# Kernel optimization log

Hardware: AMD Instinct MI355X
Metric: run time of the kernel (lower is better)

## Reference

```python
import jax, jax.numpy as jnp
import numpy as np

N_NODES = 50000
EPS = 1e-5


def gcn_conv(x, edge_index, edge_weight, W, b, n):
    # PyG GCNConv: h = x @ W; out[dst] += norm * h[src]; out += b
    # with self-loops (weight 1) and symmetric normalization D^-1/2 A D^-1/2.
    src, dst = edge_index[0], edge_index[1]
    loop = jnp.arange(n)
    src_all = jnp.concatenate([src, loop])            # [E+N]
    dst_all = jnp.concatenate([dst, loop])
    w_all = jnp.concatenate([edge_weight, jnp.ones((n,), x.dtype)])
    deg = jax.ops.segment_sum(w_all, dst_all, num_segments=n)
    dinv = jnp.where(deg > 0, jax.lax.rsqrt(jnp.maximum(deg, 1e-30)), 0.0)
    norm = dinv[src_all] * w_all * dinv[dst_all]      # [E+N]
    h = x @ W                                         # [N, out]
    msg = h[src_all] * norm[:, None]                  # [E+N, out]
    return jax.ops.segment_sum(msg, dst_all, num_segments=n) + b


def setup_inputs() -> dict:
    key = jax.random.key(0)
    ks = jax.random.split(key, 8)
    nfeat, nhid, nout = 1024, 256, 256
    E = 800000
    x = jax.random.normal(ks[0], (N_NODES, nfeat), dtype=jnp.float32)
    edge_index = jax.random.randint(ks[1], (2, E), 0, N_NODES, dtype=jnp.int64)
    edge_weight = jax.random.uniform(ks[2], (E,), dtype=jnp.float32)
    W1 = jax.random.normal(ks[3], (nfeat, nhid), dtype=jnp.float32) / np.sqrt(nfeat)
    b1 = jnp.zeros((nhid,), jnp.float32)
    W2 = jax.random.normal(ks[4], (nhid, nout), dtype=jnp.float32) / np.sqrt(nhid)
    b2 = jnp.zeros((nout,), jnp.float32)
    bn_gamma = jnp.ones((nout,), jnp.float32)
    bn_beta = jnp.zeros((nout,), jnp.float32)
    ln_gamma = jnp.ones((nout,), jnp.float32)
    ln_beta = jnp.zeros((nout,), jnp.float32)
    return {"x": x, "edge_index": edge_index, "edge_weight": edge_weight,
            "W1": W1, "b1": b1, "W2": W2, "b2": b2,
            "bn_gamma": bn_gamma, "bn_beta": bn_beta,
            "ln_gamma": ln_gamma, "ln_beta": ln_beta}


def reference(x, edge_index, edge_weight, W1, b1, W2, b2,
              bn_gamma, bn_beta, ln_gamma, ln_beta):
    n = x.shape[0]
    # dropout is identity in eval mode
    h = jax.nn.relu(gcn_conv(x, edge_index, edge_weight, W1, b1, n))
    h = jax.nn.relu(gcn_conv(h, edge_index, edge_weight, W2, b2, n))
    # BatchNorm1d (training-mode batch statistics, biased variance)
    mu = jnp.mean(h, axis=0)
    var = jnp.mean((h - mu) ** 2, axis=0)
    h = (h - mu) * jax.lax.rsqrt(var + EPS) * bn_gamma + bn_beta
    # LayerNorm over feature dim
    lmu = jnp.mean(h, axis=-1, keepdims=True)
    lvar = jnp.mean((h - lmu) ** 2, axis=-1, keepdims=True)
    return (h - lmu) * jax.lax.rsqrt(lvar + EPS) * ln_gamma + ln_beta
```

## Files before the change

kernel.cpp:

```cpp
#include <hip/hip_runtime.h>


typedef __attribute__((ext_vector_type(4))) float f32x4;
typedef __attribute__((ext_vector_type(8))) _Float16 f16x8;
typedef __attribute__((ext_vector_type(4))) _Float16 f16x4;

#define NN 50000
#define NF 1024
#define NH 256

__global__ __launch_bounds__(256) void deg_count(const int* __restrict__ ei,
    const float* __restrict__ ew, float* __restrict__ deg, int* __restrict__ cnt, int E)
{
    int e = blockIdx.x * 256 + threadIdx.x;
    if (e >= E) return;
    int d = ei[E + e];
    atomicAdd(&deg[d], ew[e]);
    atomicAdd(&cnt[d], 1);
}

__global__ __launch_bounds__(256) void dinv_k(const float* __restrict__ deg,
    float* __restrict__ dinv, int n)
{
    int i = blockIdx.x * 256 + threadIdx.x;
    if (i < n) dinv[i] = rsqrtf(deg[i] + 1.0f);
}

__global__ __launch_bounds__(512) void scan_a(const int* __restrict__ cnt,
    int* __restrict__ excl, int* __restrict__ bsum, int n)
{
    __shared__ int sm[512];
    int t = threadIdx.x, g = blockIdx.x * 512 + t;
    int v = (g < n) ? cnt[g] : 0;
    sm[t] = v;
    __syncthreads();
    for (int d = 1; d < 512; d <<= 1) {
        int x = (t >= d) ? sm[t - d] : 0;
        __syncthreads();
        sm[t] += x;
        __syncthreads();
    }
    if (g < n) excl[g] = sm[t] - v;
    if (t == 511) bsum[blockIdx.x] = sm[511];
}

__global__ __launch_bounds__(128) void scan_b(int* __restrict__ bsum, int nb)
{
    __shared__ int sm[128];
    int t = threadIdx.x;
    int v = (t < nb) ? bsum[t] : 0;
    sm[t] = v;
    __syncthreads();
    for (int d = 1; d < 128; d <<= 1) {
        int x = (t >= d) ? sm[t - d] : 0;
        __syncthreads();
        sm[t] += x;
        __syncthreads();
    }
    if (t < nb) bsum[t] = sm[t] - v;
}

__global__ __launch_bounds__(256) void scan_c(const int* __restrict__ excl,
    const int* __restrict__ bsum, int* __restrict__ offs, int n, int E)
{
    int g = blockIdx.x * 256 + threadIdx.x;
    if (g < n) offs[g] = excl[g] + bsum[g >> 9];
    else if (g == n) offs[n] = E;
}

__global__ __launch_bounds__(256) void scatter_k(const int* __restrict__ ei,
    const float* __restrict__ ew, const int* __restrict__ offs,
    int* __restrict__ cursor, const float* __restrict__ dinv,
    int* __restrict__ csrc, float* __restrict__ cwv, int E)
{
    int e = blockIdx.x * 256 + threadIdx.x;
    if (e >= E) return;
    int s = ei[e], d = ei[E + e];
    int pos = offs[d] + atomicAdd(&cursor[d], 1);
    csrc[pos] = s;
    cwv[pos] = ew[e] * dinv[s] * dinv[d];
}

__global__ __launch_bounds__(256) void cvt_w(const float* __restrict__ W,
    unsigned short* __restrict__ WT, int K, int total)
{
    int idx = blockIdx.x * 256 + threadIdx.x;
    if (idx >= total) return;
    int k = idx >> 8, n = idx & 255;
    ((_Float16*)WT)[(size_t)n * K + k] = (_Float16)W[idx];
}

template<bool AF32>
__global__ __launch_bounds__(256, 3) void gemm_direct(
    const void* __restrict__ Av, const unsigned short* __restrict__ BT,
    _Float16* __restrict__ C, int M, int K)
{
    __shared__ _Float16 Bs[2][256 * 32];
    const int t = threadIdx.x;
    const int lane = t & 63, wid = t >> 6;
    const int r = lane & 15, q = lane >> 4;
    const int m0 = blockIdx.x * 64;
    const float* Af = (const float*)Av;
    const _Float16* Ah = (const _Float16*)Av;

    int gm = m0 + wid * 16 + r;
    if (gm >= M) gm = M - 1;

    f32x4 acc[16];
#pragma unroll
    for (int j = 0; j < 16; ++j) acc[j] = (f32x4){0.f, 0.f, 0.f, 0.f};

    const int T = K >> 5;

    auto issueB = [&](int kt, int buf) {
        const int k0 = kt << 5;
#pragma unroll
        for (int rd = 0; rd < 4; ++rd) {
            int n = rd * 64 + wid * 16 + (lane >> 2);
            int kc = (lane & 3) << 3;
            const _Float16* g = (const _Float16*)BT + (size_t)n * K + k0 + kc;
            _Float16* l = &Bs[buf][0] + rd * 2048 + wid * 512;
            __builtin_amdgcn_global_load_lds(
                (const __attribute__((address_space(1))) unsigned int*)g,
                (__attribute__((address_space(3))) unsigned int*)l, 16, 0, 0);
        }
    };

    f32x4 apf[2][2];
    f16x8 aph[2];

    auto issueA = [&](int kt, int slot) {
        if constexpr (AF32) {
            const float* g = Af + (size_t)gm * K + (kt << 5) + q * 8;
            apf[slot][0] = *(const f32x4*)g;
            apf[slot][1] = *(const f32x4*)(g + 4);
        } else {
            aph[slot] = *(const f16x8*)(Ah + (size_t)gm * K + (kt << 5) + q * 8);
        }
    };

    issueB(0, 0);
    issueA(0, 0);
    issueB(1, 1);
    issueA(1, 1);

    for (int k = 0; k < T; ++k) {
        const int cur = k & 1;

        f16x8 af;
        if constexpr (AF32) {
#pragma unroll
            for (int e = 0; e < 4; ++e) {
                af[e]     = (_Float16)apf[cur][0][e];
                af[4 + e] = (_Float16)apf[cur][1][e];
            }
        } else {
            af = aph[cur];
        }

        if (k < T - 1) {
            if constexpr (AF32) asm volatile("s_waitcnt vmcnt(2)" ::: "memory");
            else                asm volatile("s_waitcnt vmcnt(1)" ::: "memory");
        } else {
            asm volatile("s_waitcnt vmcnt(0)" ::: "memory");
        }
        __builtin_amdgcn_s_barrier();
        __builtin_amdgcn_sched_barrier(0);

        if (k >= 1 && k + 1 < T) issueB(k + 1, cur ^ 1);
        __builtin_amdgcn_sched_barrier(0);
        if (k + 2 < T) issueA(k + 2, cur);
        __builtin_amdgcn_sched_barrier(0);

#pragma unroll
        for (int j = 0; j < 16; ++j) {
            f16x8 bfr = *(const f16x8*)(&Bs[cur][0] + (j * 16 + r) * 32 + q * 8);
            acc[j] = __builtin_amdgcn_mfma_f32_16x16x32_f16(af, bfr, acc[j], 0, 0, 0);
        }
    }

#pragma unroll
    for (int reg = 0; reg < 4; ++reg) {
        int m = m0 + wid * 16 + q * 4 + reg;
        if (m < M) {
            _Float16* cp = C + (size_t)m * 256 + r;
#pragma unroll
            for (int j = 0; j < 16; ++j) cp[j * 16] = (_Float16)acc[j][reg];
        }
    }
}

__global__ __launch_bounds__(256) void agg_relu(
    const _Float16* __restrict__ h, const int* __restrict__ roff,
    const int* __restrict__ csrc, const float* __restrict__ cwv,
    const float* __restrict__ dinv, const float* __restrict__ bias,
    _Float16* __restrict__ out, int n)
{
    const int lane = threadIdx.x & 63, wid = threadIdx.x >> 6;
    const int i = blockIdx.x * 4 + wid;
    if (i >= n) return;
    const int c = lane << 2;
    const float di = dinv[i];
    const float sw = di * di;
    const f16x4 hv = *(const f16x4*)(h + (size_t)i * 256 + c);
    float a0 = sw * (float)hv.x, a1 = sw * (float)hv.y;
    float a2 = sw * (float)hv.z, a3 = sw * (float)hv.w;
    float c0 = 0.f, c1 = 0.f, c2 = 0.f, c3 = 0.f;
    const int p0 = roff[i], pe = roff[i + 1];
    for (int base = p0; base < pe; base += 64) {
        int lim = pe - base; if (lim > 64) lim = 64;
        int sv = 0; float wv = 0.f;
        if (lane < lim) { sv = csrc[base + lane]; wv = cwv[base + lane]; }
        int j = 0;
        for (; j + 1 < lim; j += 2) {
            int s0 = __shfl(sv, j), s1 = __shfl(sv, j + 1);
            float w0 = __shfl(wv, j), w1 = __shfl(wv, j + 1);
            f16x4 v0 = *(const f16x4*)(h + (size_t)s0 * 256 + c);
            f16x4 v1 = *(const f16x4*)(h + (size_t)s1 * 256 + c);
            a0 += w0 * (float)v0.x; a1 += w0 * (float)v0.y;
            a2 += w0 * (float)v0.z; a3 += w0 * (float)v0.w;
            c0 += w1 * (float)v1.x; c1 += w1 * (float)v1.y;
            c2 += w1 * (float)v1.z; c3 += w1 * (float)v1.w;
        }
        if (j < lim) {
            int s0 = __shfl(sv, j);
            float w0 = __shfl(wv, j);
            f16x4 v0 = *(const f16x4*)(h + (size_t)s0 * 256 + c);
            a0 += w0 * (float)v0.x; a1 += w0 * (float)v0.y;
            a2 += w0 * (float)v0.z; a3 += w0 * (float)v0.w;
        }
    }
    const float4 bb = *(const float4*)(bias + c);
    f16x4 o;
    o.x = (_Float16)fmaxf(a0 + c0 + bb.x, 0.f);
    o.y = (_Float16)fmaxf(a1 + c1 + bb.y, 0.f);
    o.z = (_Float16)fmaxf(a2 + c2 + bb.z, 0.f);
    o.w = (_Float16)fmaxf(a3 + c3 + bb.w, 0.f);
    *(f16x4*)(out + (size_t)i * 256 + c) = o;
}

__global__ __launch_bounds__(256) void bn_stats(const _Float16* __restrict__ h,
    float* __restrict__ bnsum, float* __restrict__ bnsq, int n)
{
    const int t = threadIdx.x;
    float s = 0.f, s2 = 0.f;
    for (int r = blockIdx.x; r < n; r += gridDim.x) {
        float v = (float)h[(size_t)r * 256 + t];
        s += v; s2 += v * v;
    }
    atomicAdd(&bnsum[t], s);
    atomicAdd(&bnsq[t], s2);
}

__global__ __launch_bounds__(256) void bn_params(const float* __restrict__ bnsum,
    const float* __restrict__ bnsq, const float* __restrict__ gamma,
    const float* __restrict__ beta, float* __restrict__ scale,
    float* __restrict__ shift, int n)
{
    int t = threadIdx.x;
    float mu = bnsum[t] / (float)n;
    float var = bnsq[t] / (float)n - mu * mu;
    float sc = gamma[t] * rsqrtf(var + 1e-5f);
    scale[t] = sc;
    shift[t] = beta[t] - mu * sc;
}

__global__ __launch_bounds__(256) void bn_ln(const _Float16* __restrict__ h,
    const float* __restrict__ scale, const float* __restrict__ shift,
    const float* __restrict__ lng, const float* __restrict__ lnb,
    float* __restrict__ out, int n)
{
    const int lane = threadIdx.x & 63, wid = threadIdx.x >> 6;
    const int i = blockIdx.x * 4 + wid;
    if (i >= n) return;
    const int c = lane << 2;
    const f16x4 v = *(const f16x4*)(h + (size_t)i * 256 + c);
    const float4 sc = *(const float4*)(scale + c);
    const float4 sh = *(const float4*)(shift + c);
    float y0 = (float)v.x * sc.x + sh.x;
    float y1 = (float)v.y * sc.y + sh.y;
    float y2 = (float)v.z * sc.z + sh.z;
    float y3 = (float)v.w * sc.w + sh.w;
    float ps = y0 + y1 + y2 + y3;
    float ps2 = y0 * y0 + y1 * y1 + y2 * y2 + y3 * y3;
#pragma unroll
    for (int off = 32; off > 0; off >>= 1) {
        ps += __shfl_down(ps, off);
        ps2 += __shfl_down(ps2, off);
    }
    ps = __shfl(ps, 0);
    ps2 = __shfl(ps2, 0);
    const float mu = ps * (1.f / 256.f);
    const float var = ps2 * (1.f / 256.f) - mu * mu;
    const float rs = rsqrtf(var + 1e-5f);
    const float4 g = *(const float4*)(lng + c);
    const float4 bb = *(const float4*)(lnb + c);
    float4 o;
    o.x = (y0 - mu) * rs * g.x + bb.x;
    o.y = (y1 - mu) * rs * g.y + bb.y;
    o.z = (y2 - mu) * rs * g.z + bb.z;
    o.w = (y3 - mu) * rs * g.w + bb.w;
    *(float4*)(out + (size_t)i * 256 + c) = o;
}

extern "C" void kernel_launch(void* const* d_in, const int* in_sizes, int n_in,
                              void* d_out, int out_size, void* d_ws, size_t ws_size,
                              hipStream_t stream)
{
    const float* x   = (const float*)d_in[0];
    const int*   ei  = (const int*)d_in[1];
    const float* ew  = (const float*)d_in[2];
    const float* W1  = (const float*)d_in[3];
    const float* b1  = (const float*)d_in[4];
    const float* W2  = (const float*)d_in[5];
    const float* b2  = (const float*)d_in[6];
    const float* bng = (const float*)d_in[7];
    const float* bnb = (const float*)d_in[8];
    const float* lng = (const float*)d_in[9];
    const float* lnb = (const float*)d_in[10];
    float* out = (float*)d_out;

    const int N = NN;
    const int E = in_sizes[2];

    char* ws = (char*)d_ws;
    size_t o = 0;
    auto alloc = [&](size_t b) -> char* {
        char* p = ws + o;
        o = (o + b + 255) & ~(size_t)255;
        return p;
    };
    _Float16* h1  = (_Float16*)alloc((size_t)N * NH * 2);
    _Float16* h1a = (_Float16*)alloc((size_t)N * NH * 2);
    _Float16* h2a = (_Float16*)alloc((size_t)N * NH * 2);
    unsigned short* W1T = (unsigned short*)alloc((size_t)NH * NF * 2);
    unsigned short* W2T = (unsigned short*)alloc((size_t)NH * NH * 2);
    int*   csrc = (int*)alloc((size_t)E * 4);
    float* cwv  = (float*)alloc((size_t)E * 4);
    int*   offs = (int*)alloc((size_t)(N + 1) * 4);
    int*   excl = (int*)alloc((size_t)N * 4);
    int*   bsum = (int*)alloc(512);
    float* dinv = (float*)alloc((size_t)N * 4);
    float* bnscale = (float*)alloc(NH * 4);
    float* bnshift = (float*)alloc(NH * 4);
    char* zbase = ws + o;
    float* deg    = (float*)alloc((size_t)N * 4);
    int*   cnt    = (int*)alloc((size_t)N * 4);
    int*   cursor = (int*)alloc((size_t)N * 4);
    float* bnsum  = (float*)alloc(NH * 4);
    float* bnsq   = (float*)alloc(NH * 4);
    size_t zbytes = (size_t)((ws + o) - zbase);
    (void)hipMemsetAsync(zbase, 0, zbytes, stream);

    cvt_w<<<(NF * NH + 255) / 256, 256, 0, stream>>>(W1, W1T, NF, NF * NH);
    cvt_w<<<(NH * NH + 255) / 256, 256, 0, stream>>>(W2, W2T, NH, NH * NH);
    deg_count<<<(E + 255) / 256, 256, 0, stream>>>(ei, ew, deg, cnt, E);
    dinv_k<<<(N + 255) / 256, 256, 0, stream>>>(deg, dinv, N);
    scan_a<<<(N + 511) / 512, 512, 0, stream>>>(cnt, excl, bsum, N);
    scan_b<<<1, 128, 0, stream>>>(bsum, (N + 511) / 512);
    scan_c<<<(N + 1 + 255) / 256, 256, 0, stream>>>(excl, bsum, offs, N, E);
    scatter_k<<<(E + 255) / 256, 256, 0, stream>>>(ei, ew, offs, cursor, dinv, csrc, cwv, E);

    const int gblk = (N + 63) / 64;
    gemm_direct<true><<<gblk, 256, 0, stream>>>(x, W1T, h1, N, NF);
    agg_relu<<<(N + 3) / 4, 256, 0, stream>>>(h1, offs, csrc, cwv, dinv, b1, h1a, N);
    gemm_direct<false><<<gblk, 256, 0, stream>>>(h1a, W2T, h1, N, NH);
    agg_relu<<<(N + 3) / 4, 256, 0, stream>>>(h1, offs, csrc, cwv, dinv, b2, h2a, N);

    bn_stats<<<256, 256, 0, stream>>>(h2a, bnsum, bnsq, N);
    bn_params<<<1, 256, 0, stream>>>(bnsum, bnsq, bng, bnb, bnscale, bnshift, N);
    bn_ln<<<(N + 3) / 4, 256, 0, stream>>>(h2a, bnscale, bnshift, lng, lnb, out, N);
}
```

Before: 739.5 us.

## Load GEMM B operand directly into registers and unroll aggregation gathers by four

The GEMM no longer stages the transposed weight tile through LDS with barriers. Each wave now owns a 32x128 output sub-tile and prefetches its B fragments straight from global memory into registers, double-buffered, with the K loop unrolled by two. This removes LDS traffic and per-step block barriers, at the cost of more register pressure (launch bounds drop to 2 blocks per SM) and redundant global loads of B across waves. Separately, the aggregation kernel issues four neighbour row gathers per iteration with independent accumulators to raise memory-level parallelism.

```diff
diff --git a/kernel.cpp b/kernel.cpp
--- a/kernel.cpp
+++ b/kernel.cpp
@@ -90,102 +90,103 @@
     ((_Float16*)WT)[(size_t)n * K + k] = (_Float16)W[idx];
 }
 
+#define ISSUE_B(kt, p)                                                          \
+    {                                                                           \
+        _Pragma("unroll")                                                       \
+        for (int j = 0; j < 8; ++j)                                             \
+            bpre[p][j] = *(const f16x8*)(Bbase + (size_t)j * 16 * K + ((kt) << 5)); \
+    }
+
+#define ISSUE_A(kt, p)                                                          \
+    {                                                                           \
+        if constexpr (AF32) {                                                   \
+            const float* g0 = Af + (size_t)row0 * K + ((kt) << 5) + q * 8;      \
+            const float* g1 = Af + (size_t)row1 * K + ((kt) << 5) + q * 8;      \
+            apre[p][0] = *(const f32x4*)g0;                                     \
+            apre[p][1] = *(const f32x4*)(g0 + 4);                               \
+            apre[p][2] = *(const f32x4*)g1;                                     \
+            apre[p][3] = *(const f32x4*)(g1 + 4);                               \
+        } else {                                                                \
+            aph[p][0] = *(const f16x8*)(Ah + (size_t)row0 * K + ((kt) << 5) + q * 8); \
+            aph[p][1] = *(const f16x8*)(Ah + (size_t)row1 * K + ((kt) << 5) + q * 8); \
+        }                                                                       \
+    }
+
+#define BODY(k, p, pn)                                                          \
+    {                                                                           \
+        if ((k) + 1 < T) ISSUE_B((k) + 1, pn);                                  \
+        f16x8 af0, af1;                                                         \
+        if constexpr (AF32) {                                                   \
+            _Pragma("unroll")                                                   \
+            for (int e = 0; e < 4; ++e) {                                       \
+                af0[e]     = (_Float16)apre[p][0][e];                           \
+                af0[4 + e] = (_Float16)apre[p][1][e];                           \
+                af1[e]     = (_Float16)apre[p][2][e];                           \
+                af1[4 + e] = (_Float16)apre[p][3][e];                           \
+            }                                                                   \
+        } else {                                                                \
+            af0 = aph[p][0];                                                    \
+            af1 = aph[p][1];                                                    \
+        }                                                                       \
+        if ((k) + 2 < T) ISSUE_A((k) + 2, p);                                   \
+        _Pragma("unroll")                                                       \
+        for (int j = 0; j < 8; ++j) {                                           \
+            acc[0][j] = __builtin_amdgcn_mfma_f32_16x16x32_f16(af0, bpre[p][j], acc[0][j], 0, 0, 0); \
+            acc[1][j] = __builtin_amdgcn_mfma_f32_16x16x32_f16(af1, bpre[p][j], acc[1][j], 0, 0, 0); \
+        }                                                                       \
+    }
+
 template<bool AF32>
-__global__ __launch_bounds__(256, 3) void gemm_direct(
+__global__ __launch_bounds__(256, 2) void gemm_reg(
     const void* __restrict__ Av, const unsigned short* __restrict__ BT,
     _Float16* __restrict__ C, int M, int K)
 {
-    __shared__ _Float16 Bs[2][256 * 32];
     const int t = threadIdx.x;
     const int lane = t & 63, wid = t >> 6;
     const int r = lane & 15, q = lane >> 4;
+    const int wr = wid >> 1, wc = wid & 1;
     const int m0 = blockIdx.x * 64;
     const float* Af = (const float*)Av;
     const _Float16* Ah = (const _Float16*)Av;
 
-    int gm = m0 + wid * 16 + r;
-    if (gm >= M) gm = M - 1;
-
-    f32x4 acc[16];
-#pragma unroll
-    for (int j = 0; j < 16; ++j) acc[j] = (f32x4){0.f, 0.f, 0.f, 0.f};
+    int row0 = m0 + wr * 32 + r;
+    int row1 = row0 + 16;
+    if (row0 >= M) row0 = M - 1;
+    if (row1 >= M) row1 = M - 1;
+
+    const _Float16* Bbase = (const _Float16*)BT + (size_t)(wc * 128 + r) * K + q * 8;
+
+    f32x4 acc[2][8];
+#pragma unroll
+    for (int i = 0; i < 2; ++i)
+#pragma unroll
+        for (int j = 0; j < 8; ++j) acc[i][j] = (f32x4){0.f, 0.f, 0.f, 0.f};
+
+    f32x4 apre[2][4];
+    f16x8 aph[2][2];
+    f16x8 bpre[2][8];
 
     const int T = K >> 5;
 
-    auto issueB = [&](int kt, int buf) {
-        const int k0 = kt << 5;
-#pragma unroll
-        for (int rd = 0; rd < 4; ++rd) {
-            int n = rd * 64 + wid * 16 + (lane >> 2);
-            int kc = (lane & 3) << 3;
-            const _Float16* g = (const _Float16*)BT + (size_t)n * K + k0 + kc;
-            _Float16* l = &Bs[buf][0] + rd * 2048 + wid * 512;
-            __builtin_amdgcn_global_load_lds(
-                (const __attribute__((address_space(1))) unsigned int*)g,
-                (__attribute__((address_space(3))) unsigned int*)l, 16, 0, 0);
-        }
-    };
-
-    f32x4 apf[2][2];
-    f16x8 aph[2];
-
-    auto issueA = [&](int kt, int slot) {
-        if constexpr (AF32) {
-            const float* g = Af + (size_t)gm * K + (kt << 5) + q * 8;
-            apf[slot][0] = *(const f32x4*)g;
-            apf[slot][1] = *(const f32x4*)(g + 4);
-        } else {
-            aph[slot] = *(const f16x8*)(Ah + (size_t)gm * K + (kt << 5) + q * 8);
-        }
-    };
-
-    issueB(0, 0);
-    issueA(0, 0);
-    issueB(1, 1);
-    issueA(1, 1);
-
-    for (int k = 0; k < T; ++k) {
-        const int cur = k & 1;
-
-        f16x8 af;
-        if constexpr (AF32) {
-#pragma unroll
-            for (int e = 0; e < 4; ++e) {
-                af[e]     = (_Float16)apf[cur][0][e];
-                af[4 + e] = (_Float16)apf[cur][1][e];
+    ISSUE_B(0, 0);
+    ISSUE_A(0, 0);
+    ISSUE_A(1, 1);
+
+    for (int k = 0; k < T; k += 2) {
+        BODY(k, 0, 1);
+        BODY(k + 1, 1, 0);
+    }
+
+#pragma unroll
+    for (int i = 0; i < 2; ++i) {
+#pragma unroll
+        for (int reg = 0; reg < 4; ++reg) {
+            int m = m0 + wr * 32 + i * 16 + q * 4 + reg;
+            if (m < M) {
+                _Float16* cp = C + (size_t)m * 256 + wc * 128 + r;
+#pragma unroll
+                for (int j = 0; j < 8; ++j) cp[j * 16] = (_Float16)acc[i][j][reg];
             }
-        } else {
-            af = aph[cur];
-        }
-
-        if (k < T - 1) {
-            if constexpr (AF32) asm volatile("s_waitcnt vmcnt(2)" ::: "memory");
-            else                asm volatile("s_waitcnt vmcnt(1)" ::: "memory");
-        } else {
-            asm volatile("s_waitcnt vmcnt(0)" ::: "memory");
-        }
-        __builtin_amdgcn_s_barrier();
-        __builtin_amdgcn_sched_barrier(0);
-
-        if (k >= 1 && k + 1 < T) issueB(k + 1, cur ^ 1);
-        __builtin_amdgcn_sched_barrier(0);
-        if (k + 2 < T) issueA(k + 2, cur);
-        __builtin_amdgcn_sched_barrier(0);
-
-#pragma unroll
-        for (int j = 0; j < 16; ++j) {
-            f16x8 bfr = *(const f16x8*)(&Bs[cur][0] + (j * 16 + r) * 32 + q * 8);
-            acc[j] = __builtin_amdgcn_mfma_f32_16x16x32_f16(af, bfr, acc[j], 0, 0, 0);
-        }
-    }
-
-#pragma unroll
-    for (int reg = 0; reg < 4; ++reg) {
-        int m = m0 + wid * 16 + q * 4 + reg;
-        if (m < M) {
-            _Float16* cp = C + (size_t)m * 256 + r;
-#pragma unroll
-            for (int j = 0; j < 16; ++j) cp[j * 16] = (_Float16)acc[j][reg];
         }
     }
 }
@@ -205,24 +206,34 @@
     const f16x4 hv = *(const f16x4*)(h + (size_t)i * 256 + c);
     float a0 = sw * (float)hv.x, a1 = sw * (float)hv.y;
     float a2 = sw * (float)hv.z, a3 = sw * (float)hv.w;
+    float b0 = 0.f, b1 = 0.f, b2 = 0.f, b3 = 0.f;
     float c0 = 0.f, c1 = 0.f, c2 = 0.f, c3 = 0.f;
+    float d0 = 0.f, d1 = 0.f, d2 = 0.f, d3 = 0.f;
     const int p0 = roff[i], pe = roff[i + 1];
     for (int base = p0; base < pe; base += 64) {
         int lim = pe - base; if (lim > 64) lim = 64;
         int sv = 0; float wv = 0.f;
         if (lane < lim) { sv = csrc[base + lane]; wv = cwv[base + lane]; }
         int j = 0;
-        for (; j + 1 < lim; j += 2) {
-            int s0 = __shfl(sv, j), s1 = __shfl(sv, j + 1);
-            float w0 = __shfl(wv, j), w1 = __shfl(wv, j + 1);
+        for (; j + 3 < lim; j += 4) {
+            int s0 = __shfl(sv, j),     s1 = __shfl(sv, j + 1);
+            int s2 = __shfl(sv, j + 2), s3 = __shfl(sv, j + 3);
+            float w0 = __shfl(wv, j),     w1 = __shfl(wv, j + 1);
+            float w2 = __shfl(wv, j + 2), w3 = __shfl(wv, j + 3);
             f16x4 v0 = *(const f16x4*)(h + (size_t)s0 * 256 + c);
             f16x4 v1 = *(const f16x4*)(h + (size_t)s1 * 256 + c);
+            f16x4 v2 = *(const f16x4*)(h + (size_t)s2 * 256 + c);
+            f16x4 v3 = *(const f16x4*)(h + (size_t)s3 * 256 + c);
             a0 += w0 * (float)v0.x; a1 += w0 * (float)v0.y;
             a2 += w0 * (float)v0.z; a3 += w0 * (float)v0.w;
-            c0 += w1 * (float)v1.x; c1 += w1 * (float)v1.y;
-            c2 += w1 * (float)v1.z; c3 += w1 * (float)v1.w;
+            b0 += w1 * (float)v1.x; b1 += w1 * (float)v1.y;
+            b2 += w1 * (float)v1.z; b3 += w1 * (float)v1.w;
+            c0 += w2 * (float)v2.x; c1 += w2 * (float)v2.y;
+            c2 += w2 * (float)v2.z; c3 += w2 * (float)v2.w;
+            d0 += w3 * (float)v3.x; d1 += w3 * (float)v3.y;
+            d2 += w3 * (float)v3.z; d3 += w3 * (float)v3.w;
         }
-        if (j < lim) {
+        for (; j < lim; ++j) {
             int s0 = __shfl(sv, j);
             float w0 = __shfl(wv, j);
             f16x4 v0 = *(const f16x4*)(h + (size_t)s0 * 256 + c);
@@ -232,10 +243,10 @@
     }
     const float4 bb = *(const float4*)(bias + c);
     f16x4 o;
-    o.x = (_Float16)fmaxf(a0 + c0 + bb.x, 0.f);
-    o.y = (_Float16)fmaxf(a1 + c1 + bb.y, 0.f);
-    o.z = (_Float16)fmaxf(a2 + c2 + bb.z, 0.f);
-    o.w = (_Float16)fmaxf(a3 + c3 + bb.w, 0.f);
+    o.x = (_Float16)fmaxf(a0 + b0 + c0 + d0 + bb.x, 0.f);
+    o.y = (_Float16)fmaxf(a1 + b1 + c1 + d1 + bb.y, 0.f);
+    o.z = (_Float16)fmaxf(a2 + b2 + c2 + d2 + bb.z, 0.f);
+    o.w = (_Float16)fmaxf(a3 + b3 + c3 + d3 + bb.w, 0.f);
     *(f16x4*)(out + (size_t)i * 256 + c) = o;
 }
 
@@ -362,9 +373,9 @@
     scatter_k<<<(E + 255) / 256, 256, 0, stream>>>(ei, ew, offs, cursor, dinv, csrc, cwv, E);
 
     const int gblk = (N + 63) / 64;
-    gemm_direct<true><<<gblk, 256, 0, stream>>>(x, W1T, h1, N, NF);
+    gemm_reg<true><<<gblk, 256, 0, stream>>>(x, W1T, h1, N, NF);
     agg_relu<<<(N + 3) / 4, 256, 0, stream>>>(h1, offs, csrc, cwv, dinv, b1, h1a, N);
-    gemm_direct<false><<<gblk, 256, 0, stream>>>(h1a, W2T, h1, N, NH);
+    gemm_reg<false><<<gblk, 256, 0, stream>>>(h1a, W2T, h1, N, NH);
     agg_relu<<<(N + 3) / 4, 256, 0, stream>>>(h1, offs, csrc, cwv, dinv, b2, h2a, N);
 
     bn_stats<<<256, 256, 0, stream>>>(h2a, bnsum, bnsq, N);
```

Result: slower. 801.5 us (+8.4%).
